# Optimization experiments

Hardware: AMD Instinct MI355X
Metric: run time of the kernel (lower is better)

Reference implementation:

```python
import jax, jax.numpy as jnp
import numpy as np

HEADS = 16
DIM_HEAD = 64
SCALE = DIM_HEAD ** -0.5
MASK_VALUE = -jnp.finfo(jnp.float32).max


def setup_inputs() -> dict:
    key = jax.random.key(0)
    ks = jax.random.split(key, 6)
    b, n, dim = 2, 2048, 1024
    mem_len = 2048
    inner = HEADS * DIM_HEAD  # 1024
    return {
        "x": jax.random.normal(ks[0], (b, n, dim), jnp.float32),
        "mem_k": jax.random.normal(ks[1], (b, mem_len, inner), jnp.float32),
        "mem_v": jax.random.normal(ks[2], (b, mem_len, inner), jnp.float32),
        "pos_bias": jax.random.normal(ks[3], (HEADS, n, mem_len + n), jnp.float32) * 0.02,
        "Wq": jax.random.normal(ks[4], (dim, inner), jnp.float32) * (dim ** -0.5),
        "Wkv": jax.random.normal(ks[5], (dim, 2 * inner), jnp.float32) * (dim ** -0.5),
    }


def reference(x, mem_k, mem_v, pos_bias, Wq, Wkv):
    b, n, _ = x.shape
    # projections (note: original module returns before applying to_out)
    q = (x @ Wq) * SCALE                      # [b, n, h*d]
    k, v = jnp.split(x @ Wkv, 2, axis=-1)     # each [b, n, h*d]
    k = jnp.concatenate((mem_k, k), axis=1)   # [b, j, h*d]
    v = jnp.concatenate((mem_v, v), axis=1)

    def split_heads(t):
        return t.reshape(t.shape[0], t.shape[1], HEADS, DIM_HEAD).transpose(0, 2, 1, 3)

    q, k, v = map(split_heads, (q, k, v))     # [b, h, i/j, d]
    sim = jnp.einsum('bhid,bhjd->bhij', q, k)
    sim = sim + pos_bias[None]                # broadcast over batch
    i, j = sim.shape[-2:]
    # causal mask: triu with offset j - i + 1 is masked out
    causal_mask = jnp.triu(jnp.ones((i, j), dtype=bool), k=j - i + 1)
    sim = jnp.where(causal_mask[None, None], MASK_VALUE, sim)
    attn = jax.nn.softmax(sim, axis=-1)
    out = jnp.einsum('bhij,bhjd->bhid', attn, v)     # [b, h, i, d]
    out = out.transpose(0, 2, 1, 3).reshape(b, n, HEADS * DIM_HEAD)
    return out
```

## Files before the change

kernel.cpp:

```cpp
#include <hip/hip_runtime.h>
#include <hip/hip_bf16.h>
#include <cstdint>

#define B_     2
#define N_     2048
#define DIM_   1024
#define H_     16
#define DH_    64
#define MEM_   2048
#define JT_    4096
#define INNER_ 1024
#define SCALE_ 0.125f

typedef float f32x4 __attribute__((ext_vector_type(4)));
typedef short s16x8 __attribute__((ext_vector_type(8)));
typedef short s16x4 __attribute__((ext_vector_type(4)));

__device__ __forceinline__ short bf16_of(float f) {
    __hip_bfloat16 h = __float2bfloat16(f);
    return *(short*)&h;
}

__device__ __forceinline__ void gload16(const void* g, short* l) {
    __builtin_amdgcn_global_load_lds(
        (const __attribute__((address_space(1))) unsigned int*)g,
        (__attribute__((address_space(3))) unsigned int*)l, 16, 0, 0);
}

__global__ __launch_bounds__(256) void cast_x(
    const float* __restrict__ x, short* __restrict__ xb)
{
    const int total4 = B_ * N_ * DIM_ / 4;
    for (int idx = blockIdx.x * blockDim.x + threadIdx.x; idx < total4;
         idx += gridDim.x * blockDim.x) {
        float4 v = ((const float4*)x)[idx];
        s16x4 o;
        o[0] = bf16_of(v.x); o[1] = bf16_of(v.y);
        o[2] = bf16_of(v.z); o[3] = bf16_of(v.w);
        *(s16x4*)&xb[idx * 4] = o;
    }
}

__global__ __launch_bounds__(256) void cast_w(
    const float* __restrict__ Wq, const float* __restrict__ Wkv,
    short* __restrict__ Wt)
{
    const int kt = blockIdx.x;
    const int nt = blockIdx.y;
    __shared__ float tile[64][65];
    const int t = threadIdx.x;
    const int r = t >> 2, s4 = (t & 3) * 16;

    const int n0 = nt * 64;
    const float* src;
    int ldn, nc0;
    if (n0 < 1024) { src = Wq;  ldn = 1024; nc0 = n0; }
    else           { src = Wkv; ldn = 2048; nc0 = n0 - 1024; }
    const float scale = (n0 < 1024) ? SCALE_ : 1.0f;

#pragma unroll
    for (int kq = 0; kq < 4; ++kq) {
        float4 v = *(const float4*)&src[(size_t)(kt * 64 + r) * ldn + nc0 + s4 + kq * 4];
        tile[s4 + kq * 4 + 0][r] = v.x;
        tile[s4 + kq * 4 + 1][r] = v.y;
        tile[s4 + kq * 4 + 2][r] = v.z;
        tile[s4 + kq * 4 + 3][r] = v.w;
    }
    __syncthreads();
    short ov[16];
#pragma unroll
    for (int e = 0; e < 16; ++e) ov[e] = bf16_of(tile[r][s4 + e] * scale);
    short* dst = &Wt[(size_t)(n0 + r) * 1024 + kt * 64 + s4];
    *(s16x8*)&dst[0] = *(s16x8*)&ov[0];
    *(s16x8*)&dst[8] = *(s16x8*)&ov[8];
}

#define PLDC 152

__global__ __launch_bounds__(256) void mfma_proj(
    const short* __restrict__ Wt, const short* __restrict__ xb,
    short* __restrict__ qbuf, short* __restrict__ kbuf, short* __restrict__ vtbuf)
{
    const int bc = blockIdx.x;
    const int bi = blockIdx.y;
    const int tid = threadIdx.x;
    const int w = tid >> 6, lane = tid & 63, g = lane >> 4, li = lane & 15;
    const int wr = w >> 1, wc = w & 1;

    __shared__ short smem[128 * PLDC];
    short* A_lds = smem;
    short* B_lds = smem + 8192;

    f32x4 acc[4][4];
#pragma unroll
    for (int m = 0; m < 4; ++m)
#pragma unroll
        for (int n = 0; n < 4; ++n) acc[m][n] = f32x4{0.f, 0.f, 0.f, 0.f};

    const size_t arow0 = (size_t)bc * 128;
    const size_t brow0 = (size_t)bi * 128;

    for (int t = 0; t < 16; ++t) {
        __syncthreads();
#pragma unroll
        for (int u = 0; u < 4; ++u) {
            const int c = (w * 4 + u) * 64 + lane;
            const int row = c >> 3, q = c & 7;
            const int qs = q ^ (row & 7);
            gload16(&Wt[(arow0 + row) * 1024 + t * 64 + qs * 8],
                    &A_lds[(w * 4 + u) * 512 + lane * 8]);
            gload16(&xb[(brow0 + row) * 1024 + t * 64 + qs * 8],
                    &B_lds[(w * 4 + u) * 512 + lane * 8]);
        }
        __syncthreads();
#pragma unroll
        for (int kc = 0; kc < 2; ++kc) {
            s16x8 af[4], bf[4];
#pragma unroll
            for (int mt = 0; mt < 4; ++mt) {
                const int row = wr * 64 + mt * 16 + li;
                af[mt] = *(const s16x8*)&A_lds[row * 64 + ((kc * 4 + g) ^ (row & 7)) * 8];
            }
#pragma unroll
            for (int nt = 0; nt < 4; ++nt) {
                const int row = wc * 64 + nt * 16 + li;
                bf[nt] = *(const s16x8*)&B_lds[row * 64 + ((kc * 4 + g) ^ (row & 7)) * 8];
            }
#pragma unroll
            for (int mt = 0; mt < 4; ++mt)
#pragma unroll
                for (int nt = 0; nt < 4; ++nt)
                    acc[mt][nt] = __builtin_amdgcn_mfma_f32_16x16x32_bf16(af[mt], bf[nt], acc[mt][nt], 0, 0, 0);
        }
    }

    __syncthreads();
    const int c0 = bc * 128;
    const int i0g = bi * 128;
    const int b = i0g >> 11;
    const int ii0 = i0g & 2047;

    if (c0 < 2048) {
#pragma unroll
        for (int mt = 0; mt < 4; ++mt)
#pragma unroll
            for (int nt = 0; nt < 4; ++nt) {
                const int i_l = wc * 64 + nt * 16 + li;
                const int c_l = wr * 64 + mt * 16 + g * 4;
                s16x4 v4;
                v4[0] = bf16_of(acc[mt][nt][0]);
                v4[1] = bf16_of(acc[mt][nt][1]);
                v4[2] = bf16_of(acc[mt][nt][2]);
                v4[3] = bf16_of(acc[mt][nt][3]);
                *(s16x4*)&smem[i_l * PLDC + c_l] = v4;
            }
        __syncthreads();
        const bool isq = (c0 < 1024);
#pragma unroll
        for (int u = 0; u < 8; ++u) {
            const int ch = tid + u * 256;
            const int i_l = ch >> 4, seg = ch & 15;
            s16x8 v = *(const s16x8*)&smem[i_l * PLDC + seg * 8];
            const int cg = c0 + seg * 8;
            const int h = (cg >> 6) & 15;
            const int d = cg & 63;
            if (isq)
                *(s16x8*)&qbuf[(((size_t)(b * H_ + h)) * N_ + ii0 + i_l) * DH_ + d] = v;
            else
                *(s16x8*)&kbuf[(((size_t)(b * H_ + h)) * JT_ + MEM_ + ii0 + i_l) * DH_ + d] = v;
        }
    } else {
#pragma unroll
        for (int mt = 0; mt < 4; ++mt)
#pragma unroll
            for (int nt = 0; nt < 4; ++nt) {
                const int i_l = wc * 64 + nt * 16 + li;
                const int c_b = wr * 64 + mt * 16 + g * 4;
#pragma unroll
                for (int r = 0; r < 4; ++r)
                    smem[(c_b + r) * PLDC + i_l] = bf16_of(acc[mt][nt][r]);
            }
        __syncthreads();
#pragma unroll
        for (int u = 0; u < 8; ++u) {
            const int ch = tid + u * 256;
            const int c_l = ch >> 4, seg = ch & 15;
            s16x8 v = *(const s16x8*)&smem[c_l * PLDC + seg * 8];
            const int cv = c0 + c_l - 2048;
            const int h = cv >> 6, d = cv & 63;
            *(s16x8*)&vtbuf[(((size_t)(b * H_ + h)) * DH_ + d) * JT_ + MEM_ + ii0 + seg * 8] = v;
        }
    }
}

__global__ __launch_bounds__(256) void copymem_k(
    const float* __restrict__ mem_k, short* __restrict__ kbuf)
{
    const int total4 = B_ * MEM_ * INNER_ / 4;
    for (int idx = blockIdx.x * blockDim.x + threadIdx.x; idx < total4;
         idx += gridDim.x * blockDim.x) {
        const int flat = idx * 4;
        const int c = flat & 1023;
        const int j = (flat >> 10) & 2047;
        const int b = flat >> 21;
        const int h = c >> 6, d = c & 63;
        float4 v = ((const float4*)mem_k)[idx];
        s16x4 o;
        o[0] = bf16_of(v.x); o[1] = bf16_of(v.y);
        o[2] = bf16_of(v.z); o[3] = bf16_of(v.w);
        *(s16x4*)&kbuf[(((size_t)(b * H_ + h)) * JT_ + j) * DH_ + d] = o;
    }
}

__global__ __launch_bounds__(256) void transpose_memv(
    const float* __restrict__ mem_v, short* __restrict__ vtbuf)
{
    const int jt = blockIdx.x, h = blockIdx.y, b = blockIdx.z;
    const int j0 = jt * 64;
    __shared__ float tile[64][65];
    const int t = threadIdx.x;
    const int r = t >> 2, s4 = (t & 3) * 16;
#pragma unroll
    for (int k = 0; k < 4; ++k) {
        float4 v = *(const float4*)&mem_v[((size_t)(b * MEM_ + j0 + r)) * INNER_ + h * DH_ + s4 + k * 4];
        tile[s4 + k * 4 + 0][r] = v.x;
        tile[s4 + k * 4 + 1][r] = v.y;
        tile[s4 + k * 4 + 2][r] = v.z;
        tile[s4 + k * 4 + 3][r] = v.w;
    }
    __syncthreads();
    short ov[16];
#pragma unroll
    for (int e = 0; e < 16; ++e) ov[e] = bf16_of(tile[r][s4 + e]);
    short* dst = &vtbuf[((size_t)((b * H_ + h) * DH_ + r)) * JT_ + j0 + s4];
    *(s16x8*)&dst[0] = *(s16x8*)&ov[0];
    *(s16x8*)&dst[8] = *(s16x8*)&ov[8];
}

#define LPP 72

__global__ __launch_bounds__(256) void attn_flash(
    const short* __restrict__ qbuf, const short* __restrict__ kbuf,
    const short* __restrict__ vtbuf, const float* __restrict__ pos_bias,
    float* __restrict__ out)
{
    const int lid = blockIdx.x;
    const int k_  = lid & 255;
    const int hi  = lid >> 8;
    const int h   = (k_ & 7) | (((k_ >> 3) & 1) << 3);
    const int b   = (k_ >> 4) & 1;
    const int ztl = k_ >> 5;
    const int zt  = hi ? (15 - ztl) : ztl;
    const int i0  = zt * 128;

    const int tid = threadIdx.x;
    const int w = tid >> 6, lane = tid & 63, g = lane >> 4, li = lane & 15;

    __shared__ short K_lds[2][64 * 64];
    __shared__ short VT_lds[2][64 * 64];
    __shared__ short P_lds[4][32 * LPP];

    const size_t bh = b * H_ + h;
    const short* kg  = kbuf  + bh * (size_t)JT_ * DH_;
    const short* vtg = vtbuf + bh * (size_t)DH_ * JT_;
    const float* pb  = pos_bias + (size_t)h * N_ * JT_;

    const int qw = i0 + w * 32;

    s16x8 aq[2][2];
#pragma unroll
    for (int mt = 0; mt < 2; ++mt)
#pragma unroll
        for (int kc = 0; kc < 2; ++kc)
            aq[mt][kc] = *(const s16x8*)&qbuf[(bh * N_ + qw + mt * 16 + li) * DH_ + kc * 32 + g * 8];

    f32x4 o[2][4];
    float m_run[2], l_run[2];
#pragma unroll
    for (int mt = 0; mt < 2; ++mt) {
#pragma unroll
        for (int dt = 0; dt < 4; ++dt) o[mt][dt] = f32x4{0.f, 0.f, 0.f, 0.f};
        m_run[mt] = -3.0e38f; l_run[mt] = 0.f;
    }

    const int ntiles = 34 + 2 * zt;

    #define STAGE(bufi, j0s)                                                   \
    {                                                                          \
        _Pragma("unroll")                                                      \
        for (int u = 0; u < 2; ++u) {                                          \
            const int c = u * 256 + tid;                                       \
            const int row = c >> 3, q = c & 7;                                 \
            const int qs = q ^ (row & 7);                                      \
            gload16(&kg[(size_t)((j0s) + row) * DH_ + qs * 8],                 \
                    &K_lds[bufi][c * 8]);                                      \
            gload16(&vtg[(size_t)row * JT_ + (j0s) + qs * 8],                  \
                    &VT_lds[bufi][c * 8]);                                     \
        }                                                                      \
    }

    f32x4 bnext[2][4];
    #define LOADB(j0s)                                                         \
    {                                                                          \
        _Pragma("unroll")                                                      \
        for (int mt = 0; mt < 2; ++mt)                                         \
        _Pragma("unroll")                                                      \
        for (int nt = 0; nt < 4; ++nt)                                         \
            bnext[mt][nt] = *(const f32x4*)&pb[(size_t)(qw + mt * 16 + li) * JT_ + (j0s) + nt * 16 + g * 4]; \
    }

    STAGE(0, 0);
    LOADB(0);
    __syncthreads();

    for (int t = 0; t < ntiles; ++t) {
        const int cur = t & 1;
        const int j0 = t * 64;

        if (t + 1 < ntiles) STAGE(cur ^ 1, j0 + 64);

        f32x4 sacc[2][4];
#pragma unroll
        for (int mt = 0; mt < 2; ++mt)
#pragma unroll
            for (int nt = 0; nt < 4; ++nt) sacc[mt][nt] = bnext[mt][nt];

        if (t + 1 < ntiles) LOADB(j0 + 64);

        __builtin_amdgcn_s_setprio(1);
#pragma unroll
        for (int kc = 0; kc < 2; ++kc)
#pragma unroll
            for (int nt = 0; nt < 4; ++nt) {
                s16x8 bk = *(const s16x8*)&K_lds[cur][(nt * 16 + li) * 64 + ((kc * 4 + g) ^ (li & 7)) * 8];
                sacc[0][nt] = __builtin_amdgcn_mfma_f32_16x16x32_bf16(bk, aq[0][kc], sacc[0][nt], 0, 0, 0);
                sacc[1][nt] = __builtin_amdgcn_mfma_f32_16x16x32_bf16(bk, aq[1][kc], sacc[1][nt], 0, 0, 0);
            }
        __builtin_amdgcn_s_setprio(0);

#pragma unroll
        for (int mt = 0; mt < 2; ++mt) {
            const int q = qw + mt * 16 + li;
            if (j0 + 63 > MEM_ + qw + mt * 16) {
#pragma unroll
                for (int nt = 0; nt < 4; ++nt)
#pragma unroll
                    for (int r = 0; r < 4; ++r) {
                        const int jg = j0 + nt * 16 + g * 4 + r;
                        if (jg > MEM_ + q) sacc[mt][nt][r] = -1e30f;
                    }
            }
            float t0 = fmaxf(fmaxf(sacc[mt][0][0], sacc[mt][0][1]), fmaxf(sacc[mt][0][2], sacc[mt][0][3]));
            float t1 = fmaxf(fmaxf(sacc[mt][1][0], sacc[mt][1][1]), fmaxf(sacc[mt][1][2], sacc[mt][1][3]));
            float t2 = fmaxf(fmaxf(sacc[mt][2][0], sacc[mt][2][1]), fmaxf(sacc[mt][2][2], sacc[mt][2][3]));
            float t3 = fmaxf(fmaxf(sacc[mt][3][0], sacc[mt][3][1]), fmaxf(sacc[mt][3][2], sacc[mt][3][3]));
            float tm = fmaxf(fmaxf(t0, t1), fmaxf(t2, t3));
            tm = fmaxf(tm, __shfl_xor(tm, 16));
            tm = fmaxf(tm, __shfl_xor(tm, 32));
            const float m_new = fmaxf(m_run[mt], tm);
            const float sc = __expf(m_run[mt] - m_new);
            m_run[mt] = m_new;

#pragma unroll
            for (int nt = 0; nt < 4; ++nt)
#pragma unroll
                for (int r = 0; r < 4; ++r)
                    sacc[mt][nt][r] = __expf(sacc[mt][nt][r] - m_new);

            float s0 = (sacc[mt][0][0] + sacc[mt][0][1]) + (sacc[mt][0][2] + sacc[mt][0][3]);
            float s1 = (sacc[mt][1][0] + sacc[mt][1][1]) + (sacc[mt][1][2] + sacc[mt][1][3]);
            float s2 = (sacc[mt][2][0] + sacc[mt][2][1]) + (sacc[mt][2][2] + sacc[mt][2][3]);
            float s3 = (sacc[mt][3][0] + sacc[mt][3][1]) + (sacc[mt][3][2] + sacc[mt][3][3]);
            float ts = (s0 + s1) + (s2 + s3);
            ts += __shfl_xor(ts, 16);
            ts += __shfl_xor(ts, 32);
            l_run[mt] = l_run[mt] * sc + ts;
#pragma unroll
            for (int dt = 0; dt < 4; ++dt) o[mt][dt] *= sc;

#pragma unroll
            for (int nt = 0; nt < 4; ++nt) {
                s16x4 pk;
                pk[0] = bf16_of(sacc[mt][nt][0]);
                pk[1] = bf16_of(sacc[mt][nt][1]);
                pk[2] = bf16_of(sacc[mt][nt][2]);
                pk[3] = bf16_of(sacc[mt][nt][3]);
                *(s16x4*)&P_lds[w][(mt * 16 + li) * LPP + nt * 16 + g * 4] = pk;
            }
        }

        __builtin_amdgcn_s_setprio(1);
#pragma unroll
        for (int kc = 0; kc < 2; ++kc) {
            s16x8 pf[2];
#pragma unroll
            for (int mt = 0; mt < 2; ++mt) {
                s16x4 plo = *(const s16x4*)&P_lds[w][(mt * 16 + li) * LPP + kc * 32 + g * 8];
                s16x4 phi = *(const s16x4*)&P_lds[w][(mt * 16 + li) * LPP + kc * 32 + g * 8 + 4];
#pragma unroll
                for (int e = 0; e < 4; ++e) { pf[mt][e] = plo[e]; pf[mt][4 + e] = phi[e]; }
            }
#pragma unroll
            for (int dt = 0; dt < 4; ++dt) {
                s16x8 bv = *(const s16x8*)&VT_lds[cur][(dt * 16 + li) * 64 + ((kc * 4 + g) ^ (li & 7)) * 8];
                o[0][dt] = __builtin_amdgcn_mfma_f32_16x16x32_bf16(bv, pf[0], o[0][dt], 0, 0, 0);
                o[1][dt] = __builtin_amdgcn_mfma_f32_16x16x32_bf16(bv, pf[1], o[1][dt], 0, 0, 0);
            }
        }
        __builtin_amdgcn_s_setprio(0);

        __syncthreads();
    }
    #undef STAGE
    #undef LOADB

#pragma unroll
    for (int mt = 0; mt < 2; ++mt) {
        const float rinv = 1.0f / l_run[mt];
        const int q = qw + mt * 16 + li;
#pragma unroll
        for (int dt = 0; dt < 4; ++dt) {
            f32x4 ov = o[mt][dt] * rinv;
            *(f32x4*)&out[((size_t)(b * N_ + q)) * INNER_ + h * DH_ + dt * 16 + g * 4] = ov;
        }
    }
}

extern "C" void kernel_launch(void* const* d_in, const int* in_sizes, int n_in,
                              void* d_out, int out_size, void* d_ws, size_t ws_size,
                              hipStream_t stream)
{
    const float* x        = (const float*)d_in[0];
    const float* mem_k    = (const float*)d_in[1];
    const float* mem_v    = (const float*)d_in[2];
    const float* pos_bias = (const float*)d_in[3];
    const float* Wq       = (const float*)d_in[4];
    const float* Wkv      = (const float*)d_in[5];
    float* out = (float*)d_out;

    char* ws = (char*)d_ws;
    short* qbuf  = (short*)(ws);
    short* kbuf  = (short*)(ws + (8u << 20));
    short* vtbuf = (short*)(ws + (24u << 20));
    short* xb    = (short*)(ws + (40u << 20));
    short* Wt    = (short*)(ws + (48u << 20));

    cast_x<<<2048, 256, 0, stream>>>(x, xb);
    cast_w<<<dim3(16, 48), 256, 0, stream>>>(Wq, Wkv, Wt);
    copymem_k<<<2048, 256, 0, stream>>>(mem_k, kbuf);
    transpose_memv<<<dim3(32, H_, B_), 256, 0, stream>>>(mem_v, vtbuf);

    mfma_proj<<<dim3(24, 32), 256, 0, stream>>>(Wt, xb, qbuf, kbuf, vtbuf);

    attn_flash<<<512, 256, 0, stream>>>(qbuf, kbuf, vtbuf, pos_bias, out);
}
```

Before: 263.6 us.

## Merge memory prep kernels, add lazy softmax rescale, swizzle P tile

After: 322.3 us. 1.22x slower.

```diff
diff --git a/kernel.cpp b/kernel.cpp
--- a/kernel.cpp
+++ b/kernel.cpp
@@ -193,53 +193,51 @@
     }
 }
 
-__global__ __launch_bounds__(256) void copymem_k(
-    const float* __restrict__ mem_k, short* __restrict__ kbuf)
-{
-    const int total4 = B_ * MEM_ * INNER_ / 4;
-    for (int idx = blockIdx.x * blockDim.x + threadIdx.x; idx < total4;
-         idx += gridDim.x * blockDim.x) {
-        const int flat = idx * 4;
-        const int c = flat & 1023;
-        const int j = (flat >> 10) & 2047;
-        const int b = flat >> 21;
-        const int h = c >> 6, d = c & 63;
-        float4 v = ((const float4*)mem_k)[idx];
-        s16x4 o;
-        o[0] = bf16_of(v.x); o[1] = bf16_of(v.y);
-        o[2] = bf16_of(v.z); o[3] = bf16_of(v.w);
-        *(s16x4*)&kbuf[(((size_t)(b * H_ + h)) * JT_ + j) * DH_ + d] = o;
-    }
-}
-
-__global__ __launch_bounds__(256) void transpose_memv(
-    const float* __restrict__ mem_v, short* __restrict__ vtbuf)
-{
-    const int jt = blockIdx.x, h = blockIdx.y, b = blockIdx.z;
+__global__ __launch_bounds__(256) void prep_mem(
+    const float* __restrict__ mem_k, const float* __restrict__ mem_v,
+    short* __restrict__ kbuf, short* __restrict__ vtbuf)
+{
+    const int jt = blockIdx.x, h = blockIdx.y;
+    const int b = blockIdx.z & 1, task = blockIdx.z >> 1;
     const int j0 = jt * 64;
-    __shared__ float tile[64][65];
     const int t = threadIdx.x;
     const int r = t >> 2, s4 = (t & 3) * 16;
-#pragma unroll
-    for (int k = 0; k < 4; ++k) {
-        float4 v = *(const float4*)&mem_v[((size_t)(b * MEM_ + j0 + r)) * INNER_ + h * DH_ + s4 + k * 4];
-        tile[s4 + k * 4 + 0][r] = v.x;
-        tile[s4 + k * 4 + 1][r] = v.y;
-        tile[s4 + k * 4 + 2][r] = v.z;
-        tile[s4 + k * 4 + 3][r] = v.w;
-    }
-    __syncthreads();
-    short ov[16];
-#pragma unroll
-    for (int e = 0; e < 16; ++e) ov[e] = bf16_of(tile[r][s4 + e]);
-    short* dst = &vtbuf[((size_t)((b * H_ + h) * DH_ + r)) * JT_ + j0 + s4];
-    *(s16x8*)&dst[0] = *(s16x8*)&ov[0];
-    *(s16x8*)&dst[8] = *(s16x8*)&ov[8];
-}
-
-#define LPP 72
-
-__global__ __launch_bounds__(256) void attn_flash(
+    const size_t bh = (size_t)(b * H_ + h);
+
+    if (task == 0) {
+        short ov[16];
+#pragma unroll
+        for (int k = 0; k < 4; ++k) {
+            float4 v = *(const float4*)&mem_k[((size_t)(b * MEM_ + j0 + r)) * INNER_ + h * DH_ + s4 + k * 4];
+            ov[k * 4 + 0] = bf16_of(v.x);
+            ov[k * 4 + 1] = bf16_of(v.y);
+            ov[k * 4 + 2] = bf16_of(v.z);
+            ov[k * 4 + 3] = bf16_of(v.w);
+        }
+        short* dst = &kbuf[(bh * JT_ + j0 + r) * DH_ + s4];
+        *(s16x8*)&dst[0] = *(s16x8*)&ov[0];
+        *(s16x8*)&dst[8] = *(s16x8*)&ov[8];
+    } else {
+        __shared__ float tile[64][65];
+#pragma unroll
+        for (int k = 0; k < 4; ++k) {
+            float4 v = *(const float4*)&mem_v[((size_t)(b * MEM_ + j0 + r)) * INNER_ + h * DH_ + s4 + k * 4];
+            tile[s4 + k * 4 + 0][r] = v.x;
+            tile[s4 + k * 4 + 1][r] = v.y;
+            tile[s4 + k * 4 + 2][r] = v.z;
+            tile[s4 + k * 4 + 3][r] = v.w;
+        }
+        __syncthreads();
+        short ov[16];
+#pragma unroll
+        for (int e = 0; e < 16; ++e) ov[e] = bf16_of(tile[r][s4 + e]);
+        short* dst = &vtbuf[(bh * DH_ + r) * JT_ + j0 + s4];
+        *(s16x8*)&dst[0] = *(s16x8*)&ov[0];
+        *(s16x8*)&dst[8] = *(s16x8*)&ov[8];
+    }
+}
+
+__global__ __launch_bounds__(256, 3) void attn_flash(
     const short* __restrict__ qbuf, const short* __restrict__ kbuf,
     const short* __restrict__ vtbuf, const float* __restrict__ pos_bias,
     float* __restrict__ out)
@@ -258,9 +256,9 @@
 
     __shared__ short K_lds[2][64 * 64];
     __shared__ short VT_lds[2][64 * 64];
-    __shared__ short P_lds[4][32 * LPP];
-
-    const size_t bh = b * H_ + h;
+    __shared__ short P_lds[4][32 * 64];
+
+    const size_t bh = (size_t)(b * H_ + h);
     const short* kg  = kbuf  + bh * (size_t)JT_ * DH_;
     const short* vtg = vtbuf + bh * (size_t)DH_ * JT_;
     const float* pb  = pos_bias + (size_t)h * N_ * JT_;
@@ -316,8 +314,9 @@
     for (int t = 0; t < ntiles; ++t) {
         const int cur = t & 1;
         const int j0 = t * 64;
-
-        if (t + 1 < ntiles) STAGE(cur ^ 1, j0 + 64);
+        const bool more = (t + 1 < ntiles);
+
+        if (more) STAGE(cur ^ 1, j0 + 64);
 
         f32x4 sacc[2][4];
 #pragma unroll
@@ -325,7 +324,7 @@
 #pragma unroll
             for (int nt = 0; nt < 4; ++nt) sacc[mt][nt] = bnext[mt][nt];
 
-        if (t + 1 < ntiles) LOADB(j0 + 64);
+        if (more) LOADB(j0 + 64);
 
         __builtin_amdgcn_s_setprio(1);
 #pragma unroll
@@ -354,57 +353,55 @@
             float t1 = fmaxf(fmaxf(sacc[mt][1][0], sacc[mt][1][1]), fmaxf(sacc[mt][1][2], sacc[mt][1][3]));
             float t2 = fmaxf(fmaxf(sacc[mt][2][0], sacc[mt][2][1]), fmaxf(sacc[mt][2][2], sacc[mt][2][3]));
             float t3 = fmaxf(fmaxf(sacc[mt][3][0], sacc[mt][3][1]), fmaxf(sacc[mt][3][2], sacc[mt][3][3]));
-            float tm = fmaxf(fmaxf(t0, t1), fmaxf(t2, t3));
-            tm = fmaxf(tm, __shfl_xor(tm, 16));
-            tm = fmaxf(tm, __shfl_xor(tm, 32));
-            const float m_new = fmaxf(m_run[mt], tm);
-            const float sc = __expf(m_run[mt] - m_new);
-            m_run[mt] = m_new;
+            float tml = fmaxf(fmaxf(t0, t1), fmaxf(t2, t3));
+            if (!__all(tml <= m_run[mt] + 8.0f)) {
+                float tm = tml;
+                tm = fmaxf(tm, __shfl_xor(tm, 16));
+                tm = fmaxf(tm, __shfl_xor(tm, 32));
+                const float m_new = fmaxf(m_run[mt], tm);
+                const float sc = __expf(m_run[mt] - m_new);
+                m_run[mt] = m_new;
+                l_run[mt] *= sc;
+#pragma unroll
+                for (int dt = 0; dt < 4; ++dt) o[mt][dt] *= sc;
+            }
 
 #pragma unroll
             for (int nt = 0; nt < 4; ++nt)
 #pragma unroll
                 for (int r = 0; r < 4; ++r)
-                    sacc[mt][nt][r] = __expf(sacc[mt][nt][r] - m_new);
+                    sacc[mt][nt][r] = __expf(sacc[mt][nt][r] - m_run[mt]);
 
             float s0 = (sacc[mt][0][0] + sacc[mt][0][1]) + (sacc[mt][0][2] + sacc[mt][0][3]);
             float s1 = (sacc[mt][1][0] + sacc[mt][1][1]) + (sacc[mt][1][2] + sacc[mt][1][3]);
             float s2 = (sacc[mt][2][0] + sacc[mt][2][1]) + (sacc[mt][2][2] + sacc[mt][2][3]);
             float s3 = (sacc[mt][3][0] + sacc[mt][3][1]) + (sacc[mt][3][2] + sacc[mt][3][3]);
-            float ts = (s0 + s1) + (s2 + s3);
-            ts += __shfl_xor(ts, 16);
-            ts += __shfl_xor(ts, 32);
-            l_run[mt] = l_run[mt] * sc + ts;
-#pragma unroll
-            for (int dt = 0; dt < 4; ++dt) o[mt][dt] *= sc;
+            l_run[mt] += (s0 + s1) + (s2 + s3);
 
 #pragma unroll
             for (int nt = 0; nt < 4; ++nt) {
+                const int sl = nt * 4 + g;
+                const int gi = (sl >> 1) ^ (li & 7);
                 s16x4 pk;
                 pk[0] = bf16_of(sacc[mt][nt][0]);
                 pk[1] = bf16_of(sacc[mt][nt][1]);
                 pk[2] = bf16_of(sacc[mt][nt][2]);
                 pk[3] = bf16_of(sacc[mt][nt][3]);
-                *(s16x4*)&P_lds[w][(mt * 16 + li) * LPP + nt * 16 + g * 4] = pk;
+                *(s16x4*)&P_lds[w][(mt * 16 + li) * 64 + gi * 8 + (sl & 1) * 4] = pk;
             }
         }
 
         __builtin_amdgcn_s_setprio(1);
 #pragma unroll
         for (int kc = 0; kc < 2; ++kc) {
-            s16x8 pf[2];
-#pragma unroll
-            for (int mt = 0; mt < 2; ++mt) {
-                s16x4 plo = *(const s16x4*)&P_lds[w][(mt * 16 + li) * LPP + kc * 32 + g * 8];
-                s16x4 phi = *(const s16x4*)&P_lds[w][(mt * 16 + li) * LPP + kc * 32 + g * 8 + 4];
-#pragma unroll
-                for (int e = 0; e < 4; ++e) { pf[mt][e] = plo[e]; pf[mt][4 + e] = phi[e]; }
-            }
+            const int gir = (kc * 4 + g) ^ (li & 7);
+            s16x8 pf0 = *(const s16x8*)&P_lds[w][(0 + li) * 64 + gir * 8];
+            s16x8 pf1 = *(const s16x8*)&P_lds[w][(16 + li) * 64 + gir * 8];
 #pragma unroll
             for (int dt = 0; dt < 4; ++dt) {
                 s16x8 bv = *(const s16x8*)&VT_lds[cur][(dt * 16 + li) * 64 + ((kc * 4 + g) ^ (li & 7)) * 8];
-                o[0][dt] = __builtin_amdgcn_mfma_f32_16x16x32_bf16(bv, pf[0], o[0][dt], 0, 0, 0);
-                o[1][dt] = __builtin_amdgcn_mfma_f32_16x16x32_bf16(bv, pf[1], o[1][dt], 0, 0, 0);
+                o[0][dt] = __builtin_amdgcn_mfma_f32_16x16x32_bf16(bv, pf0, o[0][dt], 0, 0, 0);
+                o[1][dt] = __builtin_amdgcn_mfma_f32_16x16x32_bf16(bv, pf1, o[1][dt], 0, 0, 0);
             }
         }
         __builtin_amdgcn_s_setprio(0);
@@ -416,7 +413,10 @@
 
 #pragma unroll
     for (int mt = 0; mt < 2; ++mt) {
-        const float rinv = 1.0f / l_run[mt];
+        float ts = l_run[mt];
+        ts += __shfl_xor(ts, 16);
+        ts += __shfl_xor(ts, 32);
+        const float rinv = 1.0f / ts;
         const int q = qw + mt * 16 + li;
 #pragma unroll
         for (int dt = 0; dt < 4; ++dt) {
@@ -447,8 +447,7 @@
 
     cast_x<<<2048, 256, 0, stream>>>(x, xb);
     cast_w<<<dim3(16, 48), 256, 0, stream>>>(Wq, Wkv, Wt);
-    copymem_k<<<2048, 256, 0, stream>>>(mem_k, kbuf);
-    transpose_memv<<<dim3(32, H_, B_), 256, 0, stream>>>(mem_v, vtbuf);
+    prep_mem<<<dim3(32, H_, 4), 256, 0, stream>>>(mem_k, mem_v, kbuf, vtbuf);
 
     mfma_proj<<<dim3(24, 32), 256, 0, stream>>>(Wt, xb, qbuf, kbuf, vtbuf);
 
```
